# Kernel tuning notes

Hardware: AMD Instinct MI355X
Metric: run time of the kernel (lower is better)

The kernel has to match this reference:

```python
import jax, jax.numpy as jnp
from jax import lax
import numpy as np

B, T, IN, H = 512, 512, 32, 64


def _lstm_layer(x_seq, W_ih, W_hh, b_ih, b_hh):
    """One PyTorch-convention LSTM layer. x_seq: [B, T, in] -> hs: [B, T, H].
    Gate order i, f, g, o; zero initial (h, c)."""
    Bb = x_seq.shape[0]
    Hh = W_hh.shape[1]
    # Precompute input-to-gate projections for the whole sequence (one big GEMM).
    xg = jnp.einsum('bti,gi->btg', x_seq, W_ih) + b_ih + b_hh  # [B, T, 4H]

    def step(carry, xg_t):
        h, c = carry
        gates = xg_t + h @ W_hh.T  # [B, 4H]
        i, f, g, o = jnp.split(gates, 4, axis=-1)
        i = jax.nn.sigmoid(i)
        f = jax.nn.sigmoid(f)
        g = jnp.tanh(g)
        o = jax.nn.sigmoid(o)
        c = f * c + i * g
        h = o * jnp.tanh(c)
        return (h, c), h

    h0 = jnp.zeros((Bb, Hh), x_seq.dtype)
    (_, _), hs = lax.scan(step, (h0, h0), jnp.swapaxes(xg, 0, 1))  # hs: [T, B, H]
    return jnp.swapaxes(hs, 0, 1)


def setup_inputs() -> dict:
    key = jax.random.key(0)
    ks = jax.random.split(key, 11)
    s_in = 1.0 / np.sqrt(H)
    return {
        'x': jax.random.normal(ks[0], (B, T, IN), jnp.float32),
        'W_ih0': jax.random.normal(ks[1], (4 * H, IN), jnp.float32) * s_in,
        'W_hh0': jax.random.normal(ks[2], (4 * H, H), jnp.float32) * s_in,
        'b_ih0': jax.random.normal(ks[3], (4 * H,), jnp.float32) * s_in,
        'b_hh0': jax.random.normal(ks[4], (4 * H,), jnp.float32) * s_in,
        'W_ih1': jax.random.normal(ks[5], (4 * H, H), jnp.float32) * s_in,
        'W_hh1': jax.random.normal(ks[6], (4 * H, H), jnp.float32) * s_in,
        'b_ih1': jax.random.normal(ks[7], (4 * H,), jnp.float32) * s_in,
        'b_hh1': jax.random.normal(ks[8], (4 * H,), jnp.float32) * s_in,
        'W_fc': jax.random.normal(ks[9], (1, H), jnp.float32) * s_in,
        'b_fc': jax.random.normal(ks[10], (1,), jnp.float32) * s_in,
    }


def reference(x, W_ih0, W_hh0, b_ih0, b_hh0, W_ih1, W_hh1, b_ih1, b_hh1, W_fc, b_fc):
    h1 = _lstm_layer(x, W_ih0, W_hh0, b_ih0, b_hh0)   # [B, T, H]
    # inter-layer dropout and final dropout are identity in eval mode
    h2 = _lstm_layer(h1, W_ih1, W_hh1, b_ih1, b_hh1)  # [B, T, H]
    last = h2[:, -1, :]                               # [B, H]
    return last @ W_fc.T + b_fc                       # [B, 1]
```

## Files before the change

### kernel.cpp

```cpp
#include <hip/hip_runtime.h>

#define T_STEPS 512
#define BATCH   512
#define HID     64
#define NGATES  256
#define CH      32

#define PIN(x) asm volatile("" : "+v"(x))

__device__ __forceinline__ float fast_tanh(float x) {
    return 1.0f - 2.0f / (1.0f + __expf(2.0f * x));
}

template<int K_IN, bool LAST>
__global__ __launch_bounds__(256, 2)
void lstm_layer(const float* __restrict__ xin,
                const float* __restrict__ W_ih,
                const float* __restrict__ W_hh,
                const float* __restrict__ b_ih,
                const float* __restrict__ b_hh,
                float* __restrict__ hout,
                const float* __restrict__ W_fc,
                const float* __restrict__ b_fc,
                float* __restrict__ fcout)
{
    __shared__ __align__(16) float xg_s[CH * NGATES];
    __shared__ __align__(16) float xstage[CH * K_IN];
    __shared__ __align__(16) float hbuf[2][HID];

    const int b   = blockIdx.x;
    const int tid = threadIdx.x;
    const int w   = tid >> 6;
    const int l   = tid & 63;
    const int gid = l >> 4;
    const int u   = (w << 4) + (l & 15);
    const int gr  = (gid << 6) + u;

    const bool istanh = (gid == 2);
    const float sA = istanh ? 2.0f : -1.0f;
    const float sB = istanh ? 1.0f : 0.0f;
    const float sC = istanh ? -2.0f : 1.0f;

    float4 whh4[HID / 4];
    {
        const float4* hr = reinterpret_cast<const float4*>(W_hh + (size_t)gr * HID);
        #pragma unroll
        for (int k = 0; k < HID / 4; ++k) whh4[k] = hr[k];
        #pragma unroll
        for (int k = 0; k < HID / 4; ++k) {
            PIN(whh4[k].x); PIN(whh4[k].y); PIN(whh4[k].z); PIN(whh4[k].w);
        }
    }
    const float bias = b_ih[gr] + b_hh[gr];

    if (tid < 128) hbuf[tid >> 6][tid & 63] = 0.0f;
    float c = 0.0f;
    __syncthreads();

    const float* xrow = xin + (size_t)b * T_STEPS * K_IN;

    for (int c0 = 0; c0 < T_STEPS; c0 += CH) {
        {
            const float4* src = reinterpret_cast<const float4*>(xrow + c0 * K_IN);
            float4* dst = reinterpret_cast<float4*>(xstage);
            #pragma unroll
            for (int i = tid; i < CH * K_IN / 4; i += 256) dst[i] = src[i];
        }
        float4 wih4[K_IN / 4];
        {
            const float4* wr = reinterpret_cast<const float4*>(W_ih + (size_t)gr * K_IN);
            #pragma unroll
            for (int k = 0; k < K_IN / 4; ++k) wih4[k] = wr[k];
        }
        __syncthreads();

        for (int tm = 0; tm < CH; ++tm) {
            const float4* xp = reinterpret_cast<const float4*>(xstage + tm * K_IN);
            float a0 = bias, a1 = 0.0f, a2 = 0.0f, a3 = 0.0f;
            #pragma unroll
            for (int k = 0; k < K_IN / 4; ++k) {
                float4 v = xp[k];
                a0 = fmaf(wih4[k].x, v.x, a0);
                a1 = fmaf(wih4[k].y, v.y, a1);
                a2 = fmaf(wih4[k].z, v.z, a2);
                a3 = fmaf(wih4[k].w, v.w, a3);
            }
            xg_s[tm * NGATES + tid] = (a0 + a1) + (a2 + a3);
        }
        __syncthreads();

        for (int tm = 0; tm < CH; ++tm) {
            const int t = c0 + tm;
            const int p = t & 1;
            const float4* hb4 = reinterpret_cast<const float4*>(hbuf[p]);

            float a0 = xg_s[tm * NGATES + tid], a1 = 0.0f, a2 = 0.0f, a3 = 0.0f;
            #pragma unroll
            for (int k = 0; k < HID / 4; ++k) {
                float4 hv = hb4[k];
                a0 = fmaf(whh4[k].x, hv.x, a0);
                a1 = fmaf(whh4[k].y, hv.y, a1);
                a2 = fmaf(whh4[k].z, hv.z, a2);
                a3 = fmaf(whh4[k].w, hv.w, a3);
            }
            const float acc = (a0 + a1) + (a2 + a3);
            const float act = sB + sC / (1.0f + __expf(sA * acc));

            const float s1 = __shfl_xor(act, 16);
            const float s2 = __shfl_xor(act, 32);
            const float s3 = __shfl_xor(s1, 32);
            if (gid == 0) {
                c = fmaf(s1, c, act * s2);
                const float h = s3 * fast_tanh(c);
                hbuf[p ^ 1][u] = h;
                if (!LAST) hout[((size_t)b * T_STEPS + t) * HID + u] = h;
            }
            __syncthreads();
        }
    }

    if (LAST) {
        if (tid < HID) {
            float v = hbuf[0][tid] * W_fc[tid];
            #pragma unroll
            for (int off = 32; off; off >>= 1) v += __shfl_down(v, off);
            if (tid == 0) fcout[b] = v + b_fc[0];
        }
    }
}

extern "C" void kernel_launch(void* const* d_in, const int* in_sizes, int n_in,
                              void* d_out, int out_size, void* d_ws, size_t ws_size,
                              hipStream_t stream) {
    const float* x     = (const float*)d_in[0];
    const float* W_ih0 = (const float*)d_in[1];
    const float* W_hh0 = (const float*)d_in[2];
    const float* b_ih0 = (const float*)d_in[3];
    const float* b_hh0 = (const float*)d_in[4];
    const float* W_ih1 = (const float*)d_in[5];
    const float* W_hh1 = (const float*)d_in[6];
    const float* b_ih1 = (const float*)d_in[7];
    const float* b_hh1 = (const float*)d_in[8];
    const float* W_fc  = (const float*)d_in[9];
    const float* b_fc  = (const float*)d_in[10];

    float* out = (float*)d_out;
    float* h1  = (float*)d_ws;

    lstm_layer<32, false><<<BATCH, 256, 0, stream>>>(
        x, W_ih0, W_hh0, b_ih0, b_hh0, h1, nullptr, nullptr, nullptr);
    lstm_layer<64, true><<<BATCH, 256, 0, stream>>>(
        h1, W_ih1, W_hh1, b_ih1, b_hh1, nullptr, W_fc, b_fc, out);
}
```

Before: 960.2 us.

## Keep input weights in registers and broadcast activations via readlane instead of LDS

Moves the input-projection weights into per-thread registers and computes the per-step input gates for small chunks directly in registers. Each lane loads one element of x or h from memory or LDS, and the values are broadcast to the wave with readlane, replacing vector LDS reads. This removes the xg and xstage shared buffers and their barriers. Division is replaced with a hardware reciprocal, and hidden-state stores are batched per chunk. The cost is much higher register pressure from holding W_ih and W_hh per thread, which may spill or cut occupancy, and each readlane is a scalar broadcast that adds latency to the serial recurrence.

```diff
diff --git a/kernel.cpp b/kernel.cpp
--- a/kernel.cpp
+++ b/kernel.cpp
@@ -3,13 +3,16 @@
 #define T_STEPS 512
 #define BATCH   512
 #define HID     64
-#define NGATES  256
-#define CH      32
+#define CH      8
 
 #define PIN(x) asm volatile("" : "+v"(x))
 
+__device__ __forceinline__ float rlane(float v, int k) {
+    return __uint_as_float(__builtin_amdgcn_readlane(__float_as_uint(v), k));
+}
+__device__ __forceinline__ float rcpf(float x) { return __builtin_amdgcn_rcpf(x); }
 __device__ __forceinline__ float fast_tanh(float x) {
-    return 1.0f - 2.0f / (1.0f + __expf(2.0f * x));
+    return 1.0f - 2.0f * rcpf(1.0f + __expf(2.0f * x));
 }
 
 template<int K_IN, bool LAST>
@@ -24,9 +27,7 @@
                 const float* __restrict__ b_fc,
                 float* __restrict__ fcout)
 {
-    __shared__ __align__(16) float xg_s[CH * NGATES];
-    __shared__ __align__(16) float xstage[CH * K_IN];
-    __shared__ __align__(16) float hbuf[2][HID];
+    __shared__ float hbuf[2][HID];
 
     const int b   = blockIdx.x;
     const int tid = threadIdx.x;
@@ -41,15 +42,27 @@
     const float sB = istanh ? 1.0f : 0.0f;
     const float sC = istanh ? -2.0f : 1.0f;
 
-    float4 whh4[HID / 4];
+    float whh[HID];
     {
         const float4* hr = reinterpret_cast<const float4*>(W_hh + (size_t)gr * HID);
         #pragma unroll
-        for (int k = 0; k < HID / 4; ++k) whh4[k] = hr[k];
+        for (int k = 0; k < HID / 4; ++k) {
+            float4 v = hr[k];
+            whh[4*k+0] = v.x; whh[4*k+1] = v.y; whh[4*k+2] = v.z; whh[4*k+3] = v.w;
+        }
         #pragma unroll
-        for (int k = 0; k < HID / 4; ++k) {
-            PIN(whh4[k].x); PIN(whh4[k].y); PIN(whh4[k].z); PIN(whh4[k].w);
+        for (int k = 0; k < HID; ++k) PIN(whh[k]);
+    }
+    float wih[K_IN];
+    {
+        const float4* xr = reinterpret_cast<const float4*>(W_ih + (size_t)gr * K_IN);
+        #pragma unroll
+        for (int k = 0; k < K_IN / 4; ++k) {
+            float4 v = xr[k];
+            wih[4*k+0] = v.x; wih[4*k+1] = v.y; wih[4*k+2] = v.z; wih[4*k+3] = v.w;
         }
+        #pragma unroll
+        for (int k = 0; k < K_IN; ++k) PIN(wih[k]);
     }
     const float bias = b_ih[gr] + b_hh[gr];
 
@@ -58,53 +71,60 @@
     __syncthreads();
 
     const float* xrow = xin + (size_t)b * T_STEPS * K_IN;
+    float hstash[CH];
 
     for (int c0 = 0; c0 < T_STEPS; c0 += CH) {
-        {
-            const float4* src = reinterpret_cast<const float4*>(xrow + c0 * K_IN);
-            float4* dst = reinterpret_cast<float4*>(xstage);
+        float xg[CH];
+        if (K_IN == 32) {
             #pragma unroll
-            for (int i = tid; i < CH * K_IN / 4; i += 256) dst[i] = src[i];
+            for (int tm = 0; tm < CH; tm += 2) {
+                const float v = xrow[(c0 + tm) * 32 + l];
+                float a0 = bias, a1 = 0.f, a2 = 0.f, a3 = 0.f;
+                float b0 = bias, b1 = 0.f, b2 = 0.f, b3 = 0.f;
+                #pragma unroll
+                for (int k = 0; k < 32; k += 4) {
+                    a0 = fmaf(wih[k+0], rlane(v, k+0), a0);
+                    a1 = fmaf(wih[k+1], rlane(v, k+1), a1);
+                    a2 = fmaf(wih[k+2], rlane(v, k+2), a2);
+                    a3 = fmaf(wih[k+3], rlane(v, k+3), a3);
+                    b0 = fmaf(wih[k+0], rlane(v, 32+k+0), b0);
+                    b1 = fmaf(wih[k+1], rlane(v, 32+k+1), b1);
+                    b2 = fmaf(wih[k+2], rlane(v, 32+k+2), b2);
+                    b3 = fmaf(wih[k+3], rlane(v, 32+k+3), b3);
+                }
+                xg[tm]     = (a0 + a1) + (a2 + a3);
+                xg[tm + 1] = (b0 + b1) + (b2 + b3);
+            }
+        } else {
+            #pragma unroll
+            for (int tm = 0; tm < CH; ++tm) {
+                const float v = xrow[(c0 + tm) * 64 + l];
+                float a0 = bias, a1 = 0.f, a2 = 0.f, a3 = 0.f;
+                #pragma unroll
+                for (int k = 0; k < 64; k += 4) {
+                    a0 = fmaf(wih[k+0], rlane(v, k+0), a0);
+                    a1 = fmaf(wih[k+1], rlane(v, k+1), a1);
+                    a2 = fmaf(wih[k+2], rlane(v, k+2), a2);
+                    a3 = fmaf(wih[k+3], rlane(v, k+3), a3);
+                }
+                xg[tm] = (a0 + a1) + (a2 + a3);
+            }
         }
-        float4 wih4[K_IN / 4];
-        {
-            const float4* wr = reinterpret_cast<const float4*>(W_ih + (size_t)gr * K_IN);
+
+        #pragma unroll
+        for (int tm = 0; tm < CH; ++tm) {
+            const int p = (c0 + tm) & 1;
+            const float hv = hbuf[p][l];
+            float a0 = xg[tm], a1 = 0.f, a2 = 0.f, a3 = 0.f;
             #pragma unroll
-            for (int k = 0; k < K_IN / 4; ++k) wih4[k] = wr[k];
-        }
-        __syncthreads();
-
-        for (int tm = 0; tm < CH; ++tm) {
-            const float4* xp = reinterpret_cast<const float4*>(xstage + tm * K_IN);
-            float a0 = bias, a1 = 0.0f, a2 = 0.0f, a3 = 0.0f;
-            #pragma unroll
-            for (int k = 0; k < K_IN / 4; ++k) {
-                float4 v = xp[k];
-                a0 = fmaf(wih4[k].x, v.x, a0);
-                a1 = fmaf(wih4[k].y, v.y, a1);
-                a2 = fmaf(wih4[k].z, v.z, a2);
-                a3 = fmaf(wih4[k].w, v.w, a3);
-            }
-            xg_s[tm * NGATES + tid] = (a0 + a1) + (a2 + a3);
-        }
-        __syncthreads();
-
-        for (int tm = 0; tm < CH; ++tm) {
-            const int t = c0 + tm;
-            const int p = t & 1;
-            const float4* hb4 = reinterpret_cast<const float4*>(hbuf[p]);
-
-            float a0 = xg_s[tm * NGATES + tid], a1 = 0.0f, a2 = 0.0f, a3 = 0.0f;
-            #pragma unroll
-            for (int k = 0; k < HID / 4; ++k) {
-                float4 hv = hb4[k];
-                a0 = fmaf(whh4[k].x, hv.x, a0);
-                a1 = fmaf(whh4[k].y, hv.y, a1);
-                a2 = fmaf(whh4[k].z, hv.z, a2);
-                a3 = fmaf(whh4[k].w, hv.w, a3);
+            for (int k = 0; k < HID; k += 4) {
+                a0 = fmaf(whh[k+0], rlane(hv, k+0), a0);
+                a1 = fmaf(whh[k+1], rlane(hv, k+1), a1);
+                a2 = fmaf(whh[k+2], rlane(hv, k+2), a2);
+                a3 = fmaf(whh[k+3], rlane(hv, k+3), a3);
             }
             const float acc = (a0 + a1) + (a2 + a3);
-            const float act = sB + sC / (1.0f + __expf(sA * acc));
+            const float act = sB + sC * rcpf(1.0f + __expf(sA * acc));
 
             const float s1 = __shfl_xor(act, 16);
             const float s2 = __shfl_xor(act, 32);
@@ -113,9 +133,15 @@
                 c = fmaf(s1, c, act * s2);
                 const float h = s3 * fast_tanh(c);
                 hbuf[p ^ 1][u] = h;
-                if (!LAST) hout[((size_t)b * T_STEPS + t) * HID + u] = h;
+                if (!LAST) hstash[tm] = h;
             }
             __syncthreads();
+        }
+
+        if (!LAST && gid == 0) {
+            #pragma unroll
+            for (int tm = 0; tm < CH; ++tm)
+                hout[((size_t)b * T_STEPS + (c0 + tm)) * HID + u] = hstash[tm];
         }
     }
 
```

Result: slower. 1.383 ms (+44.0%).
